# Optimization experiments

Hardware: AMD Instinct MI355X
Metric: run time of the kernel (lower is better)

## Reference

```python
import jax, jax.numpy as jnp
import numpy as np

D_MODEL = 1024
NUM_HEADS = 16
D_K = D_MODEL // NUM_HEADS


def setup_inputs() -> dict:
    key = jax.random.key(0)
    ks = jax.random.split(key, 11)
    B, S, D = 2, 2048, D_MODEL
    s = 1.0 / np.sqrt(D)
    return {
        "Q": jax.random.normal(ks[0], (B, S, D), jnp.float32),
        "K": jax.random.normal(ks[1], (B, S, D), jnp.float32),
        "V": jax.random.normal(ks[2], (B, S, D), jnp.float32),
        "Wq": jax.random.normal(ks[3], (D, D), jnp.float32) * s,
        "bq": jax.random.normal(ks[4], (D,), jnp.float32) * s,
        "Wk": jax.random.normal(ks[5], (D, D), jnp.float32) * s,
        "bk": jax.random.normal(ks[6], (D,), jnp.float32) * s,
        "Wv": jax.random.normal(ks[7], (D, D), jnp.float32) * s,
        "bv": jax.random.normal(ks[8], (D,), jnp.float32) * s,
        "Wo": jax.random.normal(ks[9], (D, D), jnp.float32) * s,
        "bo": jax.random.normal(ks[10], (D,), jnp.float32) * s,
    }


def _split_heads(x):
    B, S, D = x.shape
    return x.reshape(B, S, NUM_HEADS, D_K).transpose(0, 2, 1, 3)  # [B,H,S,d_k]


def reference(Q, K, V, Wq, bq, Wk, bk, Wv, bv, Wo, bo):
    q = _split_heads(Q @ Wq + bq)
    k = _split_heads(K @ Wk + bk)
    v = _split_heads(V @ Wv + bv)
    scale = 1.0 / np.sqrt(D_K)
    scores = jnp.einsum('bhqd,bhkd->bhqk', q, k) * scale
    P = jax.nn.softmax(scores, axis=-1)  # max-subtract + exp + normalize
    O = jnp.einsum('bhqk,bhkd->bhqd', P, v)
    B, H, S, dk = O.shape
    O = O.transpose(0, 2, 1, 3).reshape(B, S, H * dk)
    return O @ Wo + bo
```

## Files before the change

kernel.cpp:

```cpp
#include <hip/hip_runtime.h>
#include <math.h>

#define S_LEN 2048
#define DMODEL 1024
#define NHEADS 16
#define DK 64

#define QSCALE 0.1803368801111244f

typedef __attribute__((ext_vector_type(8))) _Float16 f16x8;
typedef __attribute__((ext_vector_type(2))) __fp16 hf16x2;
typedef __attribute__((ext_vector_type(4))) float f32x4;

static __device__ __forceinline__ unsigned short f2h(float f) {
    _Float16 h = (_Float16)f;
    return __builtin_bit_cast(unsigned short, h);
}

static __device__ __forceinline__ unsigned pack2(float a, float b) {
    hf16x2 h = __builtin_amdgcn_cvt_pkrtz(a, b);
    return __builtin_bit_cast(unsigned, h);
}

static __device__ __forceinline__ void gload16(const void* g, void* l) {
    __builtin_amdgcn_global_load_lds(
        (const __attribute__((address_space(1))) void*)g,
        (__attribute__((address_space(3))) void*)l, 16, 0, 0);
}

__global__ __launch_bounds__(256)
void wprep_kernel(const float* __restrict__ w0, const float* __restrict__ w1,
                  const float* __restrict__ w2, const float* __restrict__ w3,
                  unsigned short* __restrict__ wt)
{
    __shared__ float tile[64][65];
    const int z = blockIdx.z;
    const float* W = z == 0 ? w0 : (z == 1 ? w1 : (z == 2 ? w2 : w3));
    unsigned short* Wt = wt + (size_t)z * 1048576;
    const int k0 = blockIdx.x * 64, n0 = blockIdx.y * 64;
    const int t = threadIdx.x;
    #pragma unroll
    for (int i = 0; i < 4; ++i) {
        int idx = i * 256 + t;
        int r = idx >> 4, c4 = (idx & 15) * 4;
        float4 v = *reinterpret_cast<const float4*>(W + (size_t)(k0 + r) * 1024 + n0 + c4);
        tile[r][c4 + 0] = v.x; tile[r][c4 + 1] = v.y;
        tile[r][c4 + 2] = v.z; tile[r][c4 + 3] = v.w;
    }
    __syncthreads();
    #pragma unroll
    for (int i = 0; i < 4; ++i) {
        int idx = i * 256 + t;
        int nr = idx >> 4, kc4 = (idx & 15) * 4;
        ushort4 h;
        h.x = f2h(tile[kc4 + 0][nr]); h.y = f2h(tile[kc4 + 1][nr]);
        h.z = f2h(tile[kc4 + 2][nr]); h.w = f2h(tile[kc4 + 3][nr]);
        *reinterpret_cast<ushort4*>(Wt + (size_t)(n0 + nr) * 1024 + k0 + kc4) = h;
    }
}

__global__ __launch_bounds__(512)
void proj_gemm_kernel(const float* __restrict__ x0, const float* __restrict__ x1,
                      const float* __restrict__ x2,
                      const unsigned short* __restrict__ wt_base,
                      const float* __restrict__ b0, const float* __restrict__ b1,
                      const float* __restrict__ b2,
                      unsigned short* __restrict__ dst_base)
{
    __shared__ char Als[16384];
    __shared__ char Bls[16384];

    const int z = blockIdx.z;
    const float* Ag = z == 0 ? x0 : (z == 1 ? x1 : x2);
    const char* Bg = (const char*)(wt_base + (size_t)z * 1048576);
    const float* bias = z == 0 ? b0 : (z == 1 ? b1 : b2);
    const int mode = z;

    const int tid = threadIdx.x;
    const int w = tid >> 6, l = tid & 63, a = l & 15, g = l >> 4;
    const int wm = w >> 2, wn = w & 3;
    const int ntile = blockIdx.y & 7;
    const int mtile = blockIdx.x + ((blockIdx.y >> 3) << 3);
    const int bm = mtile * 128, bn = ntile * 128;

    const int arow = tid >> 2;
    const int ac16 = tid & 3;
    const int aswz = (arow & 7) << 4;
    const int srow = tid >> 3;
    const int sc8 = tid & 7;

    f32x4 acc[4][2] = {};

    for (int ks = 0; ks < 16; ++ks) {
        const float* ap = Ag + (size_t)(bm + arow) * 1024 + ks * 64 + 16 * ac16;
        float4 a0 = reinterpret_cast<const float4*>(ap)[0];
        float4 a1 = reinterpret_cast<const float4*>(ap)[1];
        float4 a2 = reinterpret_cast<const float4*>(ap)[2];
        float4 a3 = reinterpret_cast<const float4*>(ap)[3];

        #pragma unroll
        for (int it = 0; it < 2; ++it) {
            const int row = it * 64 + srow;
            const int gc = (sc8 << 4) ^ ((row & 7) << 4);
            gload16(Bg + (size_t)(bn + row) * 2048 + ks * 128 + gc,
                    &Bls[(size_t)(it * 512 + tid) * 16]);
        }

        uint4 w0, w1;
        w0.x = pack2(a0.x, a0.y); w0.y = pack2(a0.z, a0.w);
        w0.z = pack2(a1.x, a1.y); w0.w = pack2(a1.z, a1.w);
        w1.x = pack2(a2.x, a2.y); w1.y = pack2(a2.z, a2.w);
        w1.z = pack2(a3.x, a3.y); w1.w = pack2(a3.z, a3.w);
        const int abase = arow * 128;
        const int aoff = 32 * ac16;
        *reinterpret_cast<uint4*>(&Als[abase + (aoff ^ aswz)]) = w0;
        *reinterpret_cast<uint4*>(&Als[abase + ((aoff + 16) ^ aswz)]) = w1;

        __syncthreads();
        #pragma unroll
        for (int kc = 0; kc < 2; ++kc) {
            f16x8 af[4], bf[2];
            #pragma unroll
            for (int mi = 0; mi < 4; ++mi) {
                const int row = wm * 64 + 16 * mi + a;
                af[mi] = *reinterpret_cast<const f16x8*>(
                    &Als[row * 128 + ((kc * 64 + g * 16) ^ ((row & 7) << 4))]);
            }
            #pragma unroll
            for (int ni = 0; ni < 2; ++ni) {
                const int row = wn * 32 + 16 * ni + a;
                bf[ni] = *reinterpret_cast<const f16x8*>(
                    &Bls[row * 128 + ((kc * 64 + g * 16) ^ ((row & 7) << 4))]);
            }
            __builtin_amdgcn_s_setprio(1);
            #pragma unroll
            for (int mi = 0; mi < 4; ++mi)
                #pragma unroll
                for (int ni = 0; ni < 2; ++ni)
                    acc[mi][ni] = __builtin_amdgcn_mfma_f32_16x16x32_f16(
                        af[mi], bf[ni], acc[mi][ni], 0, 0, 0);
            __builtin_amdgcn_s_setprio(0);
        }
        __syncthreads();
    }

    unsigned short* mydst = dst_base + (size_t)z * 4194304;

    #pragma unroll
    for (int ni = 0; ni < 2; ++ni) {
        const int n = bn + wn * 32 + 16 * ni + a;
        const float bv = bias[n];
        #pragma unroll
        for (int mi = 0; mi < 4; ++mi) {
            const int mbase = bm + wm * 64 + 16 * mi + g * 4;
            if (mode == 2) {
                const int b = mbase >> 11, s = mbase & (S_LEN - 1);
                const int h = n >> 6, d = n & (DK - 1);
                ushort4 st;
                st.x = f2h(acc[mi][ni][0] + bv);
                st.y = f2h(acc[mi][ni][1] + bv);
                st.z = f2h(acc[mi][ni][2] + bv);
                st.w = f2h(acc[mi][ni][3] + bv);
                *reinterpret_cast<ushort4*>(
                    mydst + ((size_t)((b * NHEADS + h) * DK + d)) * S_LEN + s) = st;
            } else {
                const float sc = (mode == 0) ? QSCALE : 1.0f;
                #pragma unroll
                for (int r = 0; r < 4; ++r) {
                    const int m = mbase + r;
                    const int b = m >> 11, s = m & (S_LEN - 1);
                    const int h = n >> 6, d = n & (DK - 1);
                    mydst[((size_t)((b * NHEADS + h) * S_LEN + s)) * DK + d] =
                        f2h((acc[mi][ni][r] + bv) * sc);
                }
            }
        }
    }
}

__global__ __launch_bounds__(512)
void out_gemm_kernel(const unsigned short* __restrict__ Agh,
                     const unsigned short* __restrict__ Bgh,
                     const float* __restrict__ bias, float* __restrict__ out)
{
    __shared__ char Als[16384];
    __shared__ char Bls[16384];

    const char* Ag = (const char*)Agh;
    const char* Bg = (const char*)Bgh;

    const int tid = threadIdx.x;
    const int w = tid >> 6, l = tid & 63, a = l & 15, g = l >> 4;
    const int wm = w >> 2, wn = w & 3;
    const int ntile = blockIdx.y & 7;
    const int mtile = blockIdx.x + ((blockIdx.y >> 3) << 3);
    const int bm = mtile * 128, bn = ntile * 128;

    const int srow = tid >> 3;
    const int sc8 = tid & 7;

    f32x4 acc[4][2] = {};

    for (int k0b = 0; k0b < 2048; k0b += 128) {
        #pragma unroll
        for (int it = 0; it < 2; ++it) {
            const int row = it * 64 + srow;
            const int gc = (sc8 << 4) ^ ((row & 7) << 4);
            gload16(Ag + (size_t)(bm + row) * 2048 + k0b + gc,
                    &Als[(size_t)(it * 512 + tid) * 16]);
            gload16(Bg + (size_t)(bn + row) * 2048 + k0b + gc,
                    &Bls[(size_t)(it * 512 + tid) * 16]);
        }
        __syncthreads();
        #pragma unroll
        for (int kc = 0; kc < 2; ++kc) {
            f16x8 af[4], bf[2];
            #pragma unroll
            for (int mi = 0; mi < 4; ++mi) {
                const int row = wm * 64 + 16 * mi + a;
                af[mi] = *reinterpret_cast<const f16x8*>(
                    &Als[row * 128 + ((kc * 64 + g * 16) ^ ((row & 7) << 4))]);
            }
            #pragma unroll
            for (int ni = 0; ni < 2; ++ni) {
                const int row = wn * 32 + 16 * ni + a;
                bf[ni] = *reinterpret_cast<const f16x8*>(
                    &Bls[row * 128 + ((kc * 64 + g * 16) ^ ((row & 7) << 4))]);
            }
            __builtin_amdgcn_s_setprio(1);
            #pragma unroll
            for (int mi = 0; mi < 4; ++mi)
                #pragma unroll
                for (int ni = 0; ni < 2; ++ni)
                    acc[mi][ni] = __builtin_amdgcn_mfma_f32_16x16x32_f16(
                        af[mi], bf[ni], acc[mi][ni], 0, 0, 0);
            __builtin_amdgcn_s_setprio(0);
        }
        __syncthreads();
    }

    #pragma unroll
    for (int ni = 0; ni < 2; ++ni) {
        const int n = bn + wn * 32 + 16 * ni + a;
        const float bv = bias[n];
        #pragma unroll
        for (int mi = 0; mi < 4; ++mi) {
            const int mbase = bm + wm * 64 + 16 * mi + g * 4;
            #pragma unroll
            for (int r = 0; r < 4; ++r)
                out[(size_t)(mbase + r) * 1024 + n] = acc[mi][ni][r] + bv;
        }
    }
}

__global__ __launch_bounds__(512, 4)
void attn_mfma_kernel(const unsigned short* __restrict__ qb,
                      const unsigned short* __restrict__ kb,
                      const unsigned short* __restrict__ vt,
                      unsigned short* __restrict__ ob)
{
    __shared__ char Kls[2][8192];
    __shared__ char Vls[2][8192];
    __shared__ unsigned short Pl[8][32][72];

    const int tid = threadIdx.x;
    const int w = tid >> 6;
    const int p = w >> 2;
    const int wsub = w & 3;
    const int l = tid & 63;
    const int a = l & 15;
    const int g = l >> 4;
    const int bh = blockIdx.y;
    const int q0 = blockIdx.x * 128 + wsub * 32;

    const unsigned short* qhead = qb + (size_t)bh * S_LEN * DK;
    const char* khead = (const char*)(kb + (size_t)bh * S_LEN * DK);
    const char* vhead = (const char*)(vt + (size_t)bh * DK * S_LEN);

    f16x8 qf[2][2];
    #pragma unroll
    for (int j = 0; j < 2; ++j)
        #pragma unroll
        for (int c = 0; c < 2; ++c)
            qf[j][c] = *reinterpret_cast<const f16x8*>(
                qhead + (size_t)(q0 + 16 * j + a) * DK + 32 * c + 8 * g);

    f16x8 onesf;
    #pragma unroll
    for (int i = 0; i < 8; ++i) onesf[i] = (_Float16)1.f;

    f32x4 oacc[4][2] = {};
    f32x4 lacc[2] = {};
    float mrun[2] = {-INFINITY, -INFINITY};

    const int srow = tid >> 3;
    const int sgc = ((tid & 7) << 4) ^ ((srow & 7) << 4);

    #define STAGE1(t2)                                                          \
        do {                                                                    \
            gload16(khead + (size_t)((t2) * 64 + srow) * 128 + sgc,             \
                    &Kls[(t2) & 1][(size_t)w * 1024]);                          \
            gload16(vhead + (size_t)srow * 4096 + (size_t)(t2) * 128 + sgc,     \
                    &Vls[(t2) & 1][(size_t)w * 1024]);                          \
        } while (0)

    STAGE1(0);
    STAGE1(1);
    __syncthreads();

    for (int i = 0; i < 16; ++i) {
        f16x8 kf[2][4];
        #pragma unroll
        for (int c = 0; c < 2; ++c)
            #pragma unroll
            for (int T = 0; T < 4; ++T) {
                const int row = 16 * T + a;
                kf[c][T] = *reinterpret_cast<const f16x8*>(
                    &Kls[p][row * 128 + ((64 * c + 16 * g) ^ ((row & 7) << 4))]);
            }

        #pragma unroll
        for (int j = 0; j < 2; ++j) {
            f32x4 sacc[4] = {};
            __builtin_amdgcn_s_setprio(1);
            #pragma unroll
            for (int c = 0; c < 2; ++c)
                #pragma unroll
                for (int T = 0; T < 4; ++T)
                    sacc[T] = __builtin_amdgcn_mfma_f32_16x16x32_f16(
                        kf[c][T], qf[j][c], sacc[T], 0, 0, 0);
            __builtin_amdgcn_s_setprio(0);

            float lm = -INFINITY;
            #pragma unroll
            for (int T = 0; T < 4; ++T)
                #pragma unroll
                for (int r = 0; r < 4; ++r) lm = fmaxf(lm, sacc[T][r]);

            if (!__all(lm <= mrun[j] + 8.f)) {
                float vmax = fmaxf(lm, __shfl_xor(lm, 16));
                vmax = fmaxf(vmax, __shfl_xor(vmax, 32));
                const float mnew = fmaxf(mrun[j], vmax);
                const float corr = __builtin_amdgcn_exp2f(mrun[j] - mnew);
                #pragma unroll
                for (int t = 0; t < 4; ++t) {
                    oacc[t][j][0] *= corr; oacc[t][j][1] *= corr;
                    oacc[t][j][2] *= corr; oacc[t][j][3] *= corr;
                }
                lacc[j][0] *= corr; lacc[j][1] *= corr;
                lacc[j][2] *= corr; lacc[j][3] *= corr;
                mrun[j] = mnew;
            }

            const float mj = mrun[j];
            #pragma unroll
            for (int T = 0; T < 4; ++T) {
                float e0 = __builtin_amdgcn_exp2f(sacc[T][0] - mj);
                float e1 = __builtin_amdgcn_exp2f(sacc[T][1] - mj);
                float e2 = __builtin_amdgcn_exp2f(sacc[T][2] - mj);
                float e3 = __builtin_amdgcn_exp2f(sacc[T][3] - mj);
                unsigned* dst = reinterpret_cast<unsigned*>(
                    &Pl[w][16 * j + a][16 * T + 4 * g]);
                dst[0] = pack2(e0, e1);
                dst[1] = pack2(e2, e3);
            }
        }

        f16x8 vf[2][4];
        #pragma unroll
        for (int c = 0; c < 2; ++c)
            #pragma unroll
            for (int t = 0; t < 4; ++t) {
                const int row = 16 * t + a;
                vf[c][t] = *reinterpret_cast<const f16x8*>(
                    &Vls[p][row * 128 + ((64 * c + 16 * g) ^ ((row & 7) << 4))]);
            }

        __syncthreads();
        if (i < 15) {
            STAGE1(2 * i + 2);
            STAGE1(2 * i + 3);
        }

        #pragma unroll
        for (int c = 0; c < 2; ++c) {
            f16x8 pf[2];
            #pragma unroll
            for (int j = 0; j < 2; ++j)
                pf[j] = *reinterpret_cast<const f16x8*>(
                    &Pl[w][16 * j + a][32 * c + 8 * g]);
            __builtin_amdgcn_s_setprio(1);
            #pragma unroll
            for (int t = 0; t < 4; ++t)
                #pragma unroll
                for (int j = 0; j < 2; ++j)
                    oacc[t][j] = __builtin_amdgcn_mfma_f32_16x16x32_f16(
                        vf[c][t], pf[j], oacc[t][j], 0, 0, 0);
            #pragma unroll
            for (int j = 0; j < 2; ++j)
                lacc[j] = __builtin_amdgcn_mfma_f32_16x16x32_f16(
                    onesf, pf[j], lacc[j], 0, 0, 0);
            __builtin_amdgcn_s_setprio(0);
        }
        __syncthreads();
    }
    #undef STAGE1

    float* Ob = (float*)Pl;
    float* Ml = (float*)Kls;
    if (p == 1) {
        #pragma unroll
        for (int j = 0; j < 2; ++j) {
            if (g == 0) {
                Ml[((wsub * 2 + j) * 2 + 0) * 16 + a] = mrun[j];
                Ml[((wsub * 2 + j) * 2 + 1) * 16 + a] = lacc[j][0];
            }
            #pragma unroll
            for (int t = 0; t < 4; ++t)
                #pragma unroll
                for (int r = 0; r < 4; ++r)
                    Ob[((wsub * 2 + j) * 64 + 16 * t + 4 * g + r) * 16 + a] =
                        oacc[t][j][r];
        }
    }
    __syncthreads();
    if (p == 0) {
        const int b = bh >> 4;
        const int h = bh & (NHEADS - 1);
        #pragma unroll
        for (int j = 0; j < 2; ++j) {
            const float m1 = Ml[((wsub * 2 + j) * 2 + 0) * 16 + a];
            const float l1 = Ml[((wsub * 2 + j) * 2 + 1) * 16 + a];
            const float m0 = mrun[j];
            const float ms = fmaxf(m0, m1);
            const float c0 = __builtin_amdgcn_exp2f(m0 - ms);
            const float c1 = __builtin_amdgcn_exp2f(m1 - ms);
            const float inv = 1.f / (lacc[j][0] * c0 + l1 * c1);
            unsigned short* dst0 =
                ob + (size_t)(b * S_LEN + q0 + 16 * j + a) * DMODEL + h * DK;
            #pragma unroll
            for (int t = 0; t < 4; ++t) {
                ushort4 st;
                #pragma unroll
                for (int r = 0; r < 4; ++r) {
                    const float o1 =
                        Ob[((wsub * 2 + j) * 64 + 16 * t + 4 * g + r) * 16 + a];
                    const float val = (oacc[t][j][r] * c0 + o1 * c1) * inv;
                    ((unsigned short*)&st)[r] = f2h(val);
                }
                *reinterpret_cast<ushort4*>(dst0 + 16 * t + 4 * g) = st;
            }
        }
    }
}

extern "C" void kernel_launch(void* const* d_in, const int* in_sizes, int n_in,
                              void* d_out, int out_size, void* d_ws, size_t ws_size,
                              hipStream_t stream)
{
    const float* Q  = (const float*)d_in[0];
    const float* K  = (const float*)d_in[1];
    const float* V  = (const float*)d_in[2];
    const float* Wq = (const float*)d_in[3];
    const float* bq = (const float*)d_in[4];
    const float* Wk = (const float*)d_in[5];
    const float* bk = (const float*)d_in[6];
    const float* Wv = (const float*)d_in[7];
    const float* bv = (const float*)d_in[8];
    const float* Wo = (const float*)d_in[9];
    const float* bo = (const float*)d_in[10];
    float* out = (float*)d_out;

    unsigned short* xh  = (unsigned short*)d_ws;
    unsigned short* wt  = xh + (size_t)3 * 4194304;
    unsigned short* qb  = wt + (size_t)4 * 1048576;
    unsigned short* kb  = qb + 4194304;
    unsigned short* vtb = kb + 4194304;
    unsigned short* obh = vtb + 4194304;

    wprep_kernel<<<dim3(16, 16, 4), 256, 0, stream>>>(Wq, Wk, Wv, Wo, wt);

    proj_gemm_kernel<<<dim3(8, 32, 3), 512, 0, stream>>>(
        Q, K, V, wt, bq, bk, bv, qb);

    attn_mfma_kernel<<<dim3(S_LEN / 128, 2 * NHEADS), 512, 0, stream>>>(qb, kb, vtb, obh);

    out_gemm_kernel<<<dim3(8, 32, 1), 512, 0, stream>>>(
        obh, wt + (size_t)3 * 1048576, bo, out);
}
```

Baseline: 120.8 us.

## Restructure attention loop with split K/V staging, single barrier, halved P buffer

Splits the K and V tile prefetch so K for the next iteration is double-buffered while V is loaded into a single buffer and waited on with partial vmcnt. This replaces two __syncthreads per iteration with one explicit barrier. The QK^T MFMAs for both query sub-tiles are issued together, and the P buffer is halved by reusing it sequentially for the two sub-tiles. The intent is to cut barrier stalls and shared memory use so more overlap and occupancy are possible. The cost is tighter hand-managed waitcnt ordering that is fragile, plus extra serialization through the reused P buffer.

Measured after the change: 124.0 us. 2.7% more time.

```diff
diff --git a/kernel.cpp b/kernel.cpp
--- a/kernel.cpp
+++ b/kernel.cpp
@@ -259,9 +259,9 @@
                       const unsigned short* __restrict__ vt,
                       unsigned short* __restrict__ ob)
 {
-    __shared__ char Kls[2][8192];
+    __shared__ char Kls[2][2][8192];
     __shared__ char Vls[2][8192];
-    __shared__ unsigned short Pl[8][32][72];
+    __shared__ unsigned short Pl[8][16][72];
 
     const int tid = threadIdx.x;
     const int w = tid >> 6;
@@ -293,22 +293,36 @@
     f32x4 lacc[2] = {};
     float mrun[2] = {-INFINITY, -INFINITY};
 
-    const int srow = tid >> 3;
-    const int sgc = ((tid & 7) << 4) ^ ((srow & 7) << 4);
-
-    #define STAGE1(t2)                                                          \
-        do {                                                                    \
-            gload16(khead + (size_t)((t2) * 64 + srow) * 128 + sgc,             \
-                    &Kls[(t2) & 1][(size_t)w * 1024]);                          \
-            gload16(vhead + (size_t)srow * 4096 + (size_t)(t2) * 128 + sgc,     \
-                    &Vls[(t2) & 1][(size_t)w * 1024]);                          \
+    const int sgrow = w * 8 + (l >> 3);
+    const int sgc = ((l & 7) << 4) ^ ((sgrow & 7) << 4);
+
+    #define STAGE_K(gg)                                                        \
+        do {                                                                   \
+            _Pragma("unroll")                                                  \
+            for (int t = 0; t < 2; ++t)                                        \
+                gload16(khead + (size_t)((2 * (gg) + t) * 64 + sgrow) * 128 + sgc, \
+                        &Kls[(gg) & 1][t][(size_t)w * 1024]);                  \
         } while (0)
-
-    STAGE1(0);
-    STAGE1(1);
-    __syncthreads();
+    #define STAGE_V(gg)                                                        \
+        do {                                                                   \
+            _Pragma("unroll")                                                  \
+            for (int t = 0; t < 2; ++t)                                        \
+                gload16(vhead + (size_t)sgrow * 4096 + (size_t)(2 * (gg) + t) * 128 + sgc, \
+                        &Vls[t][(size_t)w * 1024]);                            \
+        } while (0)
+
+    STAGE_K(0);
 
     for (int i = 0; i < 16; ++i) {
+        asm volatile("s_waitcnt vmcnt(0)" ::: "memory");
+        __builtin_amdgcn_sched_barrier(0);
+        __builtin_amdgcn_s_barrier();
+        __builtin_amdgcn_sched_barrier(0);
+
+        STAGE_V(i);
+        if (i < 15) STAGE_K(i + 1);
+
+        const char* Kbuf = Kls[i & 1][p];
         f16x8 kf[2][4];
         #pragma unroll
         for (int c = 0; c < 2; ++c)
@@ -316,26 +330,29 @@
             for (int T = 0; T < 4; ++T) {
                 const int row = 16 * T + a;
                 kf[c][T] = *reinterpret_cast<const f16x8*>(
-                    &Kls[p][row * 128 + ((64 * c + 16 * g) ^ ((row & 7) << 4))]);
-            }
-
+                    &Kbuf[row * 128 + ((64 * c + 16 * g) ^ ((row & 7) << 4))]);
+            }
+
+        f32x4 sacc[4][2] = {};
+        __builtin_amdgcn_s_setprio(1);
+        #pragma unroll
+        for (int c = 0; c < 2; ++c)
+            #pragma unroll
+            for (int T = 0; T < 4; ++T)
+                #pragma unroll
+                for (int j = 0; j < 2; ++j)
+                    sacc[T][j] = __builtin_amdgcn_mfma_f32_16x16x32_f16(
+                        kf[c][T], qf[j][c], sacc[T][j], 0, 0, 0);
+        __builtin_amdgcn_s_setprio(0);
+
+        float pr1[4][4];
         #pragma unroll
         for (int j = 0; j < 2; ++j) {
-            f32x4 sacc[4] = {};
-            __builtin_amdgcn_s_setprio(1);
-            #pragma unroll
-            for (int c = 0; c < 2; ++c)
-                #pragma unroll
-                for (int T = 0; T < 4; ++T)
-                    sacc[T] = __builtin_amdgcn_mfma_f32_16x16x32_f16(
-                        kf[c][T], qf[j][c], sacc[T], 0, 0, 0);
-            __builtin_amdgcn_s_setprio(0);
-
             float lm = -INFINITY;
             #pragma unroll
             for (int T = 0; T < 4; ++T)
                 #pragma unroll
-                for (int r = 0; r < 4; ++r) lm = fmaxf(lm, sacc[T][r]);
+                for (int r = 0; r < 4; ++r) lm = fmaxf(lm, sacc[T][j][r]);
 
             if (!__all(lm <= mrun[j] + 8.f)) {
                 float vmax = fmaxf(lm, __shfl_xor(lm, 16));
@@ -353,19 +370,34 @@
             }
 
             const float mj = mrun[j];
-            #pragma unroll
-            for (int T = 0; T < 4; ++T) {
-                float e0 = __builtin_amdgcn_exp2f(sacc[T][0] - mj);
-                float e1 = __builtin_amdgcn_exp2f(sacc[T][1] - mj);
-                float e2 = __builtin_amdgcn_exp2f(sacc[T][2] - mj);
-                float e3 = __builtin_amdgcn_exp2f(sacc[T][3] - mj);
-                unsigned* dst = reinterpret_cast<unsigned*>(
-                    &Pl[w][16 * j + a][16 * T + 4 * g]);
-                dst[0] = pack2(e0, e1);
-                dst[1] = pack2(e2, e3);
-            }
-        }
-
+            if (j == 0) {
+                #pragma unroll
+                for (int T = 0; T < 4; ++T) {
+                    float e0 = __builtin_amdgcn_exp2f(sacc[T][0][0] - mj);
+                    float e1 = __builtin_amdgcn_exp2f(sacc[T][0][1] - mj);
+                    float e2 = __builtin_amdgcn_exp2f(sacc[T][0][2] - mj);
+                    float e3 = __builtin_amdgcn_exp2f(sacc[T][0][3] - mj);
+                    unsigned* dst = reinterpret_cast<unsigned*>(&Pl[w][a][16 * T + 4 * g]);
+                    dst[0] = pack2(e0, e1);
+                    dst[1] = pack2(e2, e3);
+                }
+            } else {
+                #pragma unroll
+                for (int T = 0; T < 4; ++T)
+                    #pragma unroll
+                    for (int r = 0; r < 4; ++r)
+                        pr1[T][r] = __builtin_amdgcn_exp2f(sacc[T][1][r] - mj);
+            }
+        }
+
+        if (i < 15) {
+            asm volatile("s_waitcnt vmcnt(2)" ::: "memory");
+        } else {
+            asm volatile("s_waitcnt vmcnt(0)" ::: "memory");
+        }
+        __builtin_amdgcn_sched_barrier(0);
+
+        const char* Vbuf = Vls[p];
         f16x8 vf[2][4];
         #pragma unroll
         for (int c = 0; c < 2; ++c)
@@ -373,41 +405,47 @@
             for (int t = 0; t < 4; ++t) {
                 const int row = 16 * t + a;
                 vf[c][t] = *reinterpret_cast<const f16x8*>(
-                    &Vls[p][row * 128 + ((64 * c + 16 * g) ^ ((row & 7) << 4))]);
-            }
-
-        __syncthreads();
-        if (i < 15) {
-            STAGE1(2 * i + 2);
-            STAGE1(2 * i + 3);
-        }
+                    &Vbuf[row * 128 + ((64 * c + 16 * g) ^ ((row & 7) << 4))]);
+            }
 
         #pragma unroll
         for (int c = 0; c < 2; ++c) {
-            f16x8 pf[2];
-            #pragma unroll
-            for (int j = 0; j < 2; ++j)
-                pf[j] = *reinterpret_cast<const f16x8*>(
-                    &Pl[w][16 * j + a][32 * c + 8 * g]);
+            f16x8 pf = *reinterpret_cast<const f16x8*>(&Pl[w][a][32 * c + 8 * g]);
             __builtin_amdgcn_s_setprio(1);
             #pragma unroll
             for (int t = 0; t < 4; ++t)
-                #pragma unroll
-                for (int j = 0; j < 2; ++j)
-                    oacc[t][j] = __builtin_amdgcn_mfma_f32_16x16x32_f16(
-                        vf[c][t], pf[j], oacc[t][j], 0, 0, 0);
-            #pragma unroll
-            for (int j = 0; j < 2; ++j)
-                lacc[j] = __builtin_amdgcn_mfma_f32_16x16x32_f16(
-                    onesf, pf[j], lacc[j], 0, 0, 0);
+                oacc[t][0] = __builtin_amdgcn_mfma_f32_16x16x32_f16(
+                    vf[c][t], pf, oacc[t][0], 0, 0, 0);
+            lacc[0] = __builtin_amdgcn_mfma_f32_16x16x32_f16(
+                onesf, pf, lacc[0], 0, 0, 0);
             __builtin_amdgcn_s_setprio(0);
         }
-        __syncthreads();
-    }
-    #undef STAGE1
-
-    float* Ob = (float*)Pl;
-    float* Ml = (float*)Kls;
+
+        #pragma unroll
+        for (int T = 0; T < 4; ++T) {
+            unsigned* dst = reinterpret_cast<unsigned*>(&Pl[w][a][16 * T + 4 * g]);
+            dst[0] = pack2(pr1[T][0], pr1[T][1]);
+            dst[1] = pack2(pr1[T][2], pr1[T][3]);
+        }
+        #pragma unroll
+        for (int c = 0; c < 2; ++c) {
+            f16x8 pf = *reinterpret_cast<const f16x8*>(&Pl[w][a][32 * c + 8 * g]);
+            __builtin_amdgcn_s_setprio(1);
+            #pragma unroll
+            for (int t = 0; t < 4; ++t)
+                oacc[t][1] = __builtin_amdgcn_mfma_f32_16x16x32_f16(
+                    vf[c][t], pf, oacc[t][1], 0, 0, 0);
+            lacc[1] = __builtin_amdgcn_mfma_f32_16x16x32_f16(
+                onesf, pf, lacc[1], 0, 0, 0);
+            __builtin_amdgcn_s_setprio(0);
+        }
+    }
+    #undef STAGE_K
+    #undef STAGE_V
+
+    __syncthreads();
+    float* Ob = (float*)Kls;
+    float* Ml = (float*)Vls;
     if (p == 1) {
         #pragma unroll
         for (int j = 0; j < 2; ++j) {
```
